# Kernel optimization log

Measured on AMD Instinct MI355X. Metric: run time of the kernel, lower is better.

The kernel has to match this reference:

```python
import jax, jax.numpy as jnp
import numpy as np

M, NC, NT, DX = 8, 1024, 512, 3
CHUNK = 512          # chunk_size
N_STEPS = 8          # n_steps (tol=0.0 -> torch early-stop never fires)
LR = 0.1
B1, B2, EPS = 0.9, 0.999, 1e-8
SQRT5 = 5.0 ** 0.5
LOG2PI = float(np.log(2.0 * np.pi))
NOISE_LB = 1e-4      # gpytorch GreaterThan(1e-4) noise constraint


def setup_inputs():
    key = jax.random.key(0)
    k1, k2, k3 = jax.random.split(key, 3)
    return {
        "xc": jax.random.normal(k1, (M, NC, DX), jnp.float32),
        "yc": jax.random.normal(k2, (M, NC, 1), jnp.float32),
        "xt": jax.random.normal(k3, (M, NT, DX), jnp.float32),
    }


def _kernel(x1, x2, ls, outscale):
    # ScaleKernel(MaternKernel(nu=2.5)); ls: [m,1,1], outscale: [m]
    xs1, xs2 = x1 / ls, x2 / ls
    d2 = (jnp.sum(xs1 * xs1, -1)[:, :, None]
          + jnp.sum(xs2 * xs2, -1)[:, None, :]
          - 2.0 * jnp.einsum('mnd,mkd->mnk', xs1, xs2))
    d2 = jnp.clip(d2, 1e-12, None)   # clamp like gpytorch dist for grad safety
    d = jnp.sqrt(d2)
    k = (1.0 + SQRT5 * d + (5.0 / 3.0) * d2) * jnp.exp(-SQRT5 * d)
    return outscale[:, None, None] * k


def _constrained(params):
    ls = jax.nn.softplus(params["raw_ls"])                          # [m,1,1]
    outscale = jax.nn.softplus(params["raw_os"])                    # [m]
    noise = jax.nn.softplus(params["raw_noise"][:, 0]) + NOISE_LB   # [m]
    return ls, outscale, noise


def _nll(params, x, y):
    # sum over tasks of -ExactMarginalLogLikelihood (gpytorch divides by n)
    ls, outscale, noise = _constrained(params)
    n = x.shape[1]
    K = _kernel(x, x, ls, outscale) + noise[:, None, None] * jnp.eye(n, dtype=x.dtype)
    L = jnp.linalg.cholesky(K)
    diff = y - params["const"][:, None]
    alpha = jax.scipy.linalg.cho_solve((L, True), diff[..., None])[..., 0]
    quad = jnp.sum(diff * alpha, -1)
    logdet = 2.0 * jnp.sum(jnp.log(jnp.diagonal(L, axis1=-2, axis2=-1)), -1)
    mll = -0.5 * (quad + logdet + n * LOG2PI) / n
    return jnp.sum(-mll)


def _adam_step(carry, x_sub, y_sub):
    p, m_, v_, t = carry
    g = jax.grad(_nll)(p, x_sub, y_sub)
    t = t + 1.0
    tm = jax.tree_util.tree_map
    m_ = tm(lambda a, gg: B1 * a + (1.0 - B1) * gg, m_, g)
    v_ = tm(lambda a, gg: B2 * a + (1.0 - B2) * gg * gg, v_, g)
    bc1 = 1.0 - B1 ** t
    bc2 = 1.0 - B2 ** t
    p = tm(lambda pp, mm, vv: pp - LR * (mm / bc1) / (jnp.sqrt(vv / bc2) + EPS), p, m_, v_)
    return (p, m_, v_, t)


def _gp_forward(xc, yc, xt):
    y = yc[..., 0]                                    # [m, nc]
    zl = lambda s: jnp.zeros(s, jnp.float32)
    # gpytorch raw params initialize to 0
    params = {"raw_ls": zl((M, 1, 1)), "raw_os": zl((M,)),
              "raw_noise": zl((M, 1)), "const": zl((M,))}
    m_ = jax.tree_util.tree_map(jnp.zeros_like, params)
    v_ = jax.tree_util.tree_map(jnp.zeros_like, params)
    carry = (params, m_, v_, jnp.float32(0.0))
    for i in range(0, NC, CHUNK):                     # 'Expanding' strategy
        end = min(i + CHUNK, NC)
        x_sub, y_sub = xc[:, :end], y[:, :end]
        step = lambda c, _: (_adam_step(c, x_sub, y_sub), None)
        carry, _ = jax.lax.scan(step, carry, None, length=N_STEPS)
    params = carry[0]
    # posterior predictive with trained hypers (train data = full context)
    ls, outscale, noise = _constrained(params)
    Kcc = _kernel(xc, xc, ls, outscale) + noise[:, None, None] * jnp.eye(NC, dtype=xc.dtype)
    L = jnp.linalg.cholesky(Kcc)
    diff = y - params["const"][:, None]
    alpha = jax.scipy.linalg.cho_solve((L, True), diff[..., None])[..., 0]
    Ktc = _kernel(xt, xc, ls, outscale)               # [m, nt, nc]
    mean = params["const"][:, None] + jnp.einsum('mtn,mn->mt', Ktc, alpha)
    v = jax.scipy.linalg.solve_triangular(L, jnp.swapaxes(Ktc, 1, 2), lower=True)  # [m,nc,nt]
    var_f = outscale[:, None] - jnp.sum(v * v, axis=1)  # Matern(0)=1 -> prior diag = outputscale
    var = var_f + noise[:, None]                      # likelihood(f) adds observation noise
    return jnp.stack([mean, var])                     # [2, m, nt]


def reference(xc, yc, xt):
    return _gp_forward(xc, yc, xt)
```

## Files before the change

### kernel.cpp

```cpp
#include <hip/hip_runtime.h>
#include <math.h>

constexpr int MM = 8;
constexpr int NC = 1024;
constexpr int NT = 512;

constexpr size_t OFF_A     = (size_t)MM * 1024 * 1024;
constexpr size_t OFF_T     = OFF_A * 2;
constexpr size_t OFF_KTC   = OFF_T + (size_t)MM * 512 * 512;
constexpr size_t OFF_ALPHA = OFF_KTC + (size_t)MM * NT * NC;
constexpr size_t OFF_SCAL  = OFF_ALPHA + (size_t)MM * 1024;
constexpr size_t OFF_ACC   = OFF_SCAL + (size_t)MM * 32;

#define S5 2.2360679775f

__device__ __forceinline__ float sigmf(float x) { return 1.0f / (1.0f + expf(-x)); }
__device__ __forceinline__ float softplusf(float x) { return fmaxf(x, 0.0f) + log1pf(expf(-fabsf(x))); }

__device__ __forceinline__ void lt_decode(int x, int& i, int& j) {
  int ii = 0;
  while ((ii + 1) * (ii + 2) / 2 <= x) ++ii;
  i = ii; j = x - ii * (ii + 1) / 2;
}

struct SMem {
  float Ls[64 * 65];
  float Us[64 * 65];
  float Tt[32 * 33];
  float dvec[64];
  float As[16][68];
  float Bs[16][68];
  float xi[64][3];
  float xj[64][3];
  float ai[64];
  float aj[64];
  float red[4][4];
};

template <int TA, int TB>
__device__ __forceinline__ void gemm64(const float* __restrict__ A, int lda,
                                       const float* __restrict__ B, int ldb,
                                       int kBeg, int kEnd, float acc[4][4], SMem& sm) {
  int tid = threadIdx.x, tx = tid & 15, ty = tid >> 4;
  float ra[4], rb[4];
  auto ldAB = [&](int k0) {
#pragma unroll
    for (int q = 0; q < 4; ++q) {
      int e = tid + (q << 8);
      if (TA) { int kk = e >> 6, r = e & 63; ra[q] = A[(size_t)(k0 + kk) * lda + r]; }
      else    { int r = e >> 4, kk = e & 15; ra[q] = A[(size_t)r * lda + k0 + kk]; }
      if (TB) { int c = e >> 4, kk = e & 15; rb[q] = B[(size_t)c * ldb + k0 + kk]; }
      else    { int kk = e >> 6, c = e & 63; rb[q] = B[(size_t)(k0 + kk) * ldb + c]; }
    }
  };
  ldAB(kBeg);
  for (int k0 = kBeg; k0 < kEnd; k0 += 16) {
    __syncthreads();
#pragma unroll
    for (int q = 0; q < 4; ++q) {
      int e = tid + (q << 8);
      if (TA) sm.As[e >> 6][e & 63] = ra[q]; else sm.As[e & 15][e >> 4] = ra[q];
      if (TB) sm.Bs[e & 15][e >> 4] = rb[q]; else sm.Bs[e >> 6][e & 63] = rb[q];
    }
    __syncthreads();
    if (k0 + 16 < kEnd) ldAB(k0 + 16);
#pragma unroll
    for (int kk = 0; kk < 16; ++kk) {
      float a[4], b[4];
#pragma unroll
      for (int i = 0; i < 4; ++i) a[i] = sm.As[kk][ty * 4 + i];
#pragma unroll
      for (int j = 0; j < 4; ++j) b[j] = sm.Bs[kk][tx * 4 + j];
#pragma unroll
      for (int i = 0; i < 4; ++i)
#pragma unroll
        for (int j = 0; j < 4; ++j) acc[i][j] = fmaf(a[i], b[j], acc[i][j]);
    }
  }
}

__device__ void factor64(SMem& sm, float* Uout, int ldu) {
  int tid = threadIdx.x;
  int tx = tid & 15, ty = tid >> 4;
  for (int j = 0; j < 63; ++j) {
    float rinv = 1.0f / sm.Ls[j * 65 + j];
    for (int i = j + 1 + ty; i < 64; i += 16) {
      float lij = sm.Ls[i * 65 + j] * rinv;
      for (int c = j + 1 + tx; c <= i; c += 16) sm.Ls[i * 65 + c] -= lij * sm.Ls[c * 65 + j];
    }
    __syncthreads();
  }
  if (tid < 64) sm.dvec[tid] = 1.0f / sqrtf(sm.Ls[tid * 65 + tid]);
  __syncthreads();
  for (int e = tid; e < 4096; e += 256) { int r = e >> 6, c = e & 63; if (c <= r) sm.Ls[r * 65 + c] *= sm.dvec[c]; }
  __syncthreads();
  for (int e = tid; e < 64 * 65; e += 256) sm.Us[e] = 0.0f;
  __syncthreads();
  if (tid < 64) {
    int b = tid >> 5, c0 = tid & 31, base = b * 32, gc = base + c0;
    sm.Us[gc * 65 + gc] = 1.0f / sm.Ls[gc * 65 + gc];
    for (int r = c0 + 1; r < 32; ++r) {
      int gr = base + r;
      float acc = 0.0f;
      for (int l = c0; l < r; ++l) acc += sm.Ls[gr * 65 + base + l] * sm.Us[(base + l) * 65 + gc];
      sm.Us[gr * 65 + gc] = -acc / sm.Ls[gr * 65 + gr];
    }
  }
  __syncthreads();
  for (int e = tid; e < 1024; e += 256) {
    int r = e >> 5, c = e & 31;
    float acc = 0.0f;
    for (int l = c; l < 32; ++l) acc += sm.Ls[(32 + r) * 65 + l] * sm.Us[l * 65 + c];
    sm.Tt[r * 33 + c] = acc;
  }
  __syncthreads();
  for (int e = tid; e < 1024; e += 256) {
    int r = e >> 5, c = e & 31;
    float acc = 0.0f;
    for (int l = 0; l <= r; ++l) acc += sm.Us[(32 + r) * 65 + 32 + l] * sm.Tt[l * 33 + c];
    sm.Us[(32 + r) * 65 + c] = -acc;
  }
  __syncthreads();
  for (int e = tid; e < 4096; e += 256) { int r = e >> 6, c = e & 63; Uout[(size_t)r * ldu + c] = sm.Us[r * 65 + c]; }
}


__global__ __launch_bounds__(256) void k_init(float* ws) {
  int t = threadIdx.x;
  float* scal = ws + OFF_SCAL;
  float* acc = ws + OFF_ACC;
  if (t < MM) {
    float* s = scal + t * 32;
    for (int i = 0; i < 12; ++i) s[i] = 0.0f;
    float sp0 = 0.69314718056f;
    s[12] = sp0; s[13] = sp0; s[14] = sp0 + 1e-4f; s[15] = 0.0f;
  }
  if (t < MM * 8) acc[t] = 0.0f;
}

__global__ __launch_bounds__(256) void k_adam(const float* __restrict__ yc, float* ws,
                                              int pn, int tstep) {
  int m = blockIdx.x, tid = threadIdx.x;
  float* sT = ws + OFF_SCAL + m * 32;
  float* accp = ws + OFF_ACC + m * 8;
  const float* al = ws + OFF_ALPHA + (size_t)m * 1024;
  const float* ym = yc + (size_t)m * NC;
  __shared__ float red[4][4];
  float cm = sT[15];
  float t4 = 0, t5 = 0, t6 = 0;
  for (int i = tid; i < pn; i += 256) {
    float a = al[i];
    t4 = fmaf(a, a, t4); t5 += a; t6 = fmaf(ym[i] - cm, a, t6);
  }
  for (int off = 32; off; off >>= 1) {
    t4 += __shfl_down(t4, off); t5 += __shfl_down(t5, off); t6 += __shfl_down(t6, off);
  }
  int wid = tid >> 6, lane = tid & 63;
  if (lane == 0) { red[wid][0] = t4; red[wid][1] = t5; red[wid][2] = t6; }
  __syncthreads();
  if (tid == 0) {
    t4 = red[0][0] + red[1][0] + red[2][0] + red[3][0];
    t5 = red[0][1] + red[1][1] + red[2][1] + red[3][1];
    t6 = red[0][2] + red[1][2] + red[2][2] + red[3][2];
    float T1 = accp[0], T2 = accp[1], t3 = accp[2];
    float ls = sT[12], os = sT[13], noi = sT[14];
    float fn = (float)pn;
    float g_ls = 0.5f / fn * (T1 - T2);
    float g_os = 0.5f / (fn * os) * (fn - noi * t3 - t6 + noi * t4);
    float g_no = 0.5f / fn * (t3 - t4);
    float g_c = -t5 / fn;
    float gr[4];
    gr[0] = g_ls * sigmf(sT[0]);
    gr[1] = g_os * sigmf(sT[1]);
    gr[2] = g_no * sigmf(sT[2]);
    gr[3] = g_c;
    float bc1 = 1.0f - powf(0.9f, (float)tstep);
    float bc2 = 1.0f - powf(0.999f, (float)tstep);
#pragma unroll
    for (int i = 0; i < 4; ++i) {
      float mv = 0.9f * sT[4 + i] + 0.1f * gr[i];
      float vv = 0.999f * sT[8 + i] + 0.001f * gr[i] * gr[i];
      sT[4 + i] = mv; sT[8 + i] = vv;
      sT[i] = sT[i] - 0.1f * (mv / bc1) / (sqrtf(vv / bc2) + 1e-8f);
    }
    sT[12] = softplusf(sT[0]);
    sT[13] = softplusf(sT[1]);
    sT[14] = softplusf(sT[2]) + 1e-4f;
    sT[15] = sT[3];
  }
}

__global__ __launch_bounds__(256) void k_buildK(const float* __restrict__ xc, float* ws, int n) {
  __shared__ SMem sm;
  int job = blockIdx.x, m = blockIdx.y, tid = threadIdx.x;
  const float* xm = xc + (size_t)m * NC * 3;
  float* Km = ws + (size_t)m * 1048576;
  float* Am = ws + OFF_A + (size_t)m * 1048576;
  const float* sT = ws + OFF_SCAL + m * 32;
  float ls = sT[12], os = sT[13], noi = sT[14];
  float il2 = 1.0f / (ls * ls);
  if (job >= 1 && job <= 4) {
    int zi = (job - 1) * 256 + tid;
    if (zi < n) ws[OFF_ALPHA + (size_t)m * 1024 + zi] = 0.0f;
  }
  if (job == 5 && tid < 4) ws[OFF_ACC + m * 8 + tid] = 0.0f;
  int bi, bj; lt_decode(job, bi, bj);
  if (tid < 64) {
    int r = bi * 64 + tid;
    sm.xi[tid][0] = xm[r * 3 + 0]; sm.xi[tid][1] = xm[r * 3 + 1]; sm.xi[tid][2] = xm[r * 3 + 2];
  } else if (tid < 128) {
    int lr = tid - 64; int r = bj * 64 + lr;
    sm.xj[lr][0] = xm[r * 3 + 0]; sm.xj[lr][1] = xm[r * 3 + 1]; sm.xj[lr][2] = xm[r * 3 + 2];
  }
  __syncthreads();
  if (job == 0) {
    for (int e = tid; e < 4096; e += 256) {
      int r = e >> 6, c = e & 63;
      float d0 = sm.xi[r][0] - sm.xj[c][0], d1 = sm.xi[r][1] - sm.xj[c][1], d2 = sm.xi[r][2] - sm.xj[c][2];
      float r2 = d0 * d0 + d1 * d1 + d2 * d2;
      float z = fmaxf(r2 * il2, 1e-12f);
      float dd = sqrtf(z);
      float kv = os * (1.0f + S5 * dd + (5.0f / 3.0f) * z) * expf(-S5 * dd);
      if (r == c) kv += noi;
      sm.Ls[r * 65 + c] = kv;
    }
    __syncthreads();
    factor64(sm, Am, n);
  } else {
    for (int e = tid; e < 4096; e += 256) {
      int r = e >> 6, c = e & 63;
      float d0 = sm.xi[r][0] - sm.xj[c][0], d1 = sm.xi[r][1] - sm.xj[c][1], d2 = sm.xi[r][2] - sm.xj[c][2];
      float r2 = d0 * d0 + d1 * d1 + d2 * d2;
      float z = fmaxf(r2 * il2, 1e-12f);
      float dd = sqrtf(z);
      float kv = os * (1.0f + S5 * dd + (5.0f / 3.0f) * z) * expf(-S5 * dd);
      if (bi == bj && r == c) kv += noi;
      Km[(size_t)(bi * 64 + r) * n + bj * 64 + c] = kv;
    }
  }
}

__global__ __launch_bounds__(256) void k_trail(float* ws, int k, int n) {
  __shared__ SMem sm;
  int job = blockIdx.x, m = blockIdx.y, tid = threadIdx.x;
  int tx = tid & 15, ty = tid >> 4;
  float* Km = ws + (size_t)m * 1048576;
  float* Am = ws + OFF_A + (size_t)m * 1048576;
  const float* Linv = Am + (size_t)(k * 64) * n + k * 64;
  int di, dj; lt_decode(job, di, dj);
  int i = k + 1 + di, j = k + 1 + dj;
  float pp[4][4] = {};
  gemm64<0, 1>(Km + (size_t)(i * 64) * n + k * 64, n, Linv, n, 0, 64, pp, sm);
  __syncthreads();
#pragma unroll
  for (int ii = 0; ii < 4; ++ii)
#pragma unroll
    for (int jj = 0; jj < 4; ++jj) sm.Ls[(ty * 4 + ii) * 65 + tx * 4 + jj] = pp[ii][jj];
  if (di == dj) {
    float* P = Am + (size_t)(i * 64) * n + k * 64;
#pragma unroll
    for (int ii = 0; ii < 4; ++ii)
#pragma unroll
      for (int jj = 0; jj < 4; ++jj) P[(size_t)(ty * 4 + ii) * n + tx * 4 + jj] = pp[ii][jj];
  } else {
#pragma unroll
    for (int ii = 0; ii < 4; ++ii)
#pragma unroll
      for (int jj = 0; jj < 4; ++jj) pp[ii][jj] = 0.0f;
    gemm64<0, 1>(Km + (size_t)(j * 64) * n + k * 64, n, Linv, n, 0, 64, pp, sm);
#pragma unroll
    for (int ii = 0; ii < 4; ++ii)
#pragma unroll
      for (int jj = 0; jj < 4; ++jj) sm.Us[(ty * 4 + ii) * 65 + tx * 4 + jj] = pp[ii][jj];
  }
  __syncthreads();
  float acc[4][4] = {};
  {
    const float* Bsrc = (di == dj) ? sm.Ls : sm.Us;
    for (int l = 0; l < 64; ++l) {
      float a[4], b[4];
#pragma unroll
      for (int ii = 0; ii < 4; ++ii) a[ii] = sm.Ls[(ty * 4 + ii) * 65 + l];
#pragma unroll
      for (int jj = 0; jj < 4; ++jj) b[jj] = Bsrc[(tx * 4 + jj) * 65 + l];
#pragma unroll
      for (int ii = 0; ii < 4; ++ii)
#pragma unroll
        for (int jj = 0; jj < 4; ++jj) acc[ii][jj] = fmaf(a[ii], b[jj], acc[ii][jj]);
    }
  }
  float* C = Km + (size_t)(i * 64) * n + j * 64;
  if (job == 0) {
    __syncthreads();
#pragma unroll
    for (int ii = 0; ii < 4; ++ii)
#pragma unroll
      for (int jj = 0; jj < 4; ++jj)
        sm.Ls[(ty * 4 + ii) * 65 + tx * 4 + jj] =
            C[(size_t)(ty * 4 + ii) * n + tx * 4 + jj] - acc[ii][jj];
    __syncthreads();
    factor64(sm, Am + (size_t)((k + 1) * 64) * n + (k + 1) * 64, n);
  } else {
#pragma unroll
    for (int ii = 0; ii < 4; ++ii)
#pragma unroll
      for (int jj = 0; jj < 4; ++jj)
        C[(size_t)(ty * 4 + ii) * n + tx * 4 + jj] -= acc[ii][jj];
  }
}

__global__ __launch_bounds__(256) void k_trinv64(float* ws, int n) {
  __shared__ SMem sm;
  int p = blockIdx.x, m = blockIdx.y, tid = threadIdx.x;
  int tx = tid & 15, ty = tid >> 4;
  float* Am = ws + OFF_A + (size_t)m * 1048576;
  int rb = (2 * p + 1) * 64, cb = 2 * p * 64;
  for (int e = tid; e < 4096; e += 256) {
    int r = e >> 6, c = e & 63;
    sm.Ls[r * 65 + c] = Am[(size_t)(rb + r) * n + cb + c];
    sm.Us[r * 65 + c] = Am[(size_t)(cb + r) * n + cb + c];
  }
  __syncthreads();
  float tt[4][4] = {};
  for (int l = 0; l < 64; ++l) {
    float a[4], b[4];
#pragma unroll
    for (int ii = 0; ii < 4; ++ii) a[ii] = sm.Ls[(ty * 4 + ii) * 65 + l];
#pragma unroll
    for (int jj = 0; jj < 4; ++jj) b[jj] = sm.Us[l * 65 + tx * 4 + jj];
#pragma unroll
    for (int ii = 0; ii < 4; ++ii)
#pragma unroll
      for (int jj = 0; jj < 4; ++jj) tt[ii][jj] = fmaf(a[ii], b[jj], tt[ii][jj]);
  }
  __syncthreads();
#pragma unroll
  for (int ii = 0; ii < 4; ++ii)
#pragma unroll
    for (int jj = 0; jj < 4; ++jj) sm.Ls[(ty * 4 + ii) * 65 + tx * 4 + jj] = tt[ii][jj];
  for (int e = tid; e < 4096; e += 256) {
    int r = e >> 6, c = e & 63;
    sm.Us[r * 65 + c] = Am[(size_t)(rb + r) * n + rb + c];
  }
  __syncthreads();
  float oo[4][4] = {};
  for (int l = 0; l < 64; ++l) {
    float a[4], b[4];
#pragma unroll
    for (int ii = 0; ii < 4; ++ii) a[ii] = sm.Us[(ty * 4 + ii) * 65 + l];
#pragma unroll
    for (int jj = 0; jj < 4; ++jj) b[jj] = sm.Ls[l * 65 + tx * 4 + jj];
#pragma unroll
    for (int ii = 0; ii < 4; ++ii)
#pragma unroll
      for (int jj = 0; jj < 4; ++jj) oo[ii][jj] = fmaf(a[ii], b[jj], oo[ii][jj]);
  }
#pragma unroll
  for (int ii = 0; ii < 4; ++ii)
#pragma unroll
    for (int jj = 0; jj < 4; ++jj)
      Am[(size_t)(rb + ty * 4 + ii) * n + cb + tx * 4 + jj] = -oo[ii][jj];
}

__global__ __launch_bounds__(256) void k_trinvT(float* ws, int s, int n) {
  __shared__ SMem sm;
  int job = blockIdx.x, m = blockIdx.y;
  int tx = threadIdx.x & 15, ty = threadIdx.x >> 4;
  float* Am = ws + OFF_A + (size_t)m * 1048576;
  float* Tm = ws + OFF_T + (size_t)m * 262144;
  int st = s >> 6;
  int p = job / (st * st), rem = job % (st * st);
  int ti = rem / st, tj = rem % st;
  int base = p * 2 * s;
  float acc[4][4] = {};
  gemm64<0, 0>(Am + (size_t)(base + s + ti * 64) * n + base, n,
               Am + (size_t)base * n + base + tj * 64, n, tj * 64, s, acc, sm);
  float* C = Tm + (size_t)p * s * s + (size_t)(ti * 64) * s + tj * 64;
#pragma unroll
  for (int ii = 0; ii < 4; ++ii)
#pragma unroll
    for (int jj = 0; jj < 4; ++jj) C[(size_t)(ty * 4 + ii) * s + tx * 4 + jj] = acc[ii][jj];
}

__global__ __launch_bounds__(256) void k_trinvA(float* ws, int s, int n) {
  __shared__ SMem sm;
  int job = blockIdx.x, m = blockIdx.y;
  int tx = threadIdx.x & 15, ty = threadIdx.x >> 4;
  float* Am = ws + OFF_A + (size_t)m * 1048576;
  const float* Tm = ws + OFF_T + (size_t)m * 262144;
  int st = s >> 6;
  int p = job / (st * st), rem = job % (st * st);
  int ti = rem / st, tj = rem % st;
  int base = p * 2 * s;
  float acc[4][4] = {};
  gemm64<0, 0>(Am + (size_t)(base + s + ti * 64) * n + base + s, n,
               Tm + (size_t)p * s * s + tj * 64, s, 0, (ti + 1) * 64, acc, sm);
  float* C = Am + (size_t)(base + s + ti * 64) * n + base + tj * 64;
#pragma unroll
  for (int ii = 0; ii < 4; ++ii)
#pragma unroll
    for (int jj = 0; jj < 4; ++jj) C[(size_t)(ty * 4 + ii) * n + tx * 4 + jj] = -acc[ii][jj];
}

__global__ __launch_bounds__(256) void k_syrkAT(const float* __restrict__ yc, float* ws, int n) {
  __shared__ SMem sm;
  int job = blockIdx.x, m = blockIdx.y, tid = threadIdx.x;
  int tx = tid & 15, ty = tid >> 4;
  const float* Am = ws + OFF_A + (size_t)m * 1048576;
  float* Gm = ws + (size_t)m * 1048576;
  const float* ym = yc + (size_t)m * NC;
  float* accp = ws + OFF_ACC + m * 8;
  float* al = ws + OFF_ALPHA + (size_t)m * 1024;
  float cm = ws[OFF_SCAL + m * 32 + 15];
  int ib, jb; lt_decode(job, ib, jb);
  if (tid < 64) sm.ai[tid] = ym[ib * 64 + tid] - cm;
  else if (tid < 128) sm.aj[tid - 64] = ym[jb * 64 + tid - 64] - cm;
  float acc[4][4] = {};
  gemm64<1, 0>(Am + ib * 64, n, Am + jb * 64, n, ib * 64, n, acc, sm);
#pragma unroll
  for (int ii = 0; ii < 4; ++ii)
#pragma unroll
    for (int jj = 0; jj < 4; ++jj) {
      int r = ty * 4 + ii, c = tx * 4 + jj;
      Gm[(size_t)(ib * 64 + r) * n + jb * 64 + c] = acc[ii][jj];
      if (ib != jb) Gm[(size_t)(jb * 64 + c) * n + ib * 64 + r] = acc[ii][jj];
    }
  if (ib == jb && tx == ty) {
    atomicAdd(&accp[2], acc[0][0] + acc[1][1] + acc[2][2] + acc[3][3]);
  }
  float rowp[4];
#pragma unroll
  for (int i = 0; i < 4; ++i) {
    float s = 0.0f;
#pragma unroll
    for (int j = 0; j < 4; ++j) s = fmaf(acc[i][j], sm.aj[tx * 4 + j], s);
    rowp[i] = s;
  }
  float colp[4];
  if (ib != jb) {
#pragma unroll
    for (int j = 0; j < 4; ++j) {
      float s = 0.0f;
#pragma unroll
      for (int i = 0; i < 4; ++i) s = fmaf(acc[i][j], sm.ai[ty * 4 + i], s);
      colp[j] = s;
    }
  }
  __syncthreads();
  float* redA = &sm.As[0][0];
  float* redB = &sm.Bs[0][0];
#pragma unroll
  for (int i = 0; i < 4; ++i) redA[(ty * 4 + i) * 16 + tx] = rowp[i];
  if (ib != jb) {
#pragma unroll
    for (int j = 0; j < 4; ++j) redB[(tx * 4 + j) * 16 + ty] = colp[j];
  }
  __syncthreads();
  if (tid < 64) {
    float s = 0.0f;
#pragma unroll
    for (int q = 0; q < 16; ++q) s += redA[tid * 16 + q];
    atomicAdd(&al[ib * 64 + tid], s);
    if (ib != jb) {
      float s2 = 0.0f;
#pragma unroll
      for (int q = 0; q < 16; ++q) s2 += redB[tid * 16 + q];
      atomicAdd(&al[jb * 64 + tid], s2);
    }
  }
}

__global__ __launch_bounds__(256) void k_reduce(const float* __restrict__ xc, float* ws, int n) {
  __shared__ SMem sm;
  int job = blockIdx.x, m = blockIdx.y, tid = threadIdx.x;
  const float* xm = xc + (size_t)m * NC * 3;
  const float* Gm = ws + (size_t)m * 1048576;
  const float* al = ws + OFF_ALPHA + (size_t)m * 1024;
  float* accp = ws + OFF_ACC + m * 8;
  const float* sT = ws + OFF_SCAL + m * 32;
  float ls = sT[12], os = sT[13];
  float il2 = 1.0f / (ls * ls);
  float c53 = (5.0f / 3.0f) * os / ls;
  int bi, bj; lt_decode(job, bi, bj);
  float w = (bi == bj) ? 1.0f : 2.0f;
  if (tid < 64) {
    int r = bi * 64 + tid;
    sm.xi[tid][0] = xm[r * 3 + 0]; sm.xi[tid][1] = xm[r * 3 + 1]; sm.xi[tid][2] = xm[r * 3 + 2];
    sm.ai[tid] = al[r];
  } else if (tid < 128) {
    int lr = tid - 64; int r = bj * 64 + lr;
    sm.xj[lr][0] = xm[r * 3 + 0]; sm.xj[lr][1] = xm[r * 3 + 1]; sm.xj[lr][2] = xm[r * 3 + 2];
    sm.aj[lr] = al[r];
  }
  __syncthreads();
  float a1 = 0.0f, a2 = 0.0f;
  for (int e = tid; e < 4096; e += 256) {
    int r = e >> 6, c = e & 63;
    float d0 = sm.xi[r][0] - sm.xj[c][0], d1 = sm.xi[r][1] - sm.xj[c][1], d2 = sm.xi[r][2] - sm.xj[c][2];
    float r2 = d0 * d0 + d1 * d1 + d2 * d2;
    float z = fmaxf(r2 * il2, 1e-12f);
    float dd = sqrtf(z);
    float Cv = c53 * z * (1.0f + S5 * dd) * expf(-S5 * dd);
    float g = Gm[(size_t)(bi * 64 + r) * n + bj * 64 + c];
    a1 = fmaf(g, Cv, a1);
    a2 = fmaf(sm.ai[r] * sm.aj[c], Cv, a2);
  }
  a1 *= w; a2 *= w;
  for (int off = 32; off; off >>= 1) { a1 += __shfl_down(a1, off); a2 += __shfl_down(a2, off); }
  int wid = tid >> 6, lane = tid & 63;
  if (lane == 0) { sm.red[wid][0] = a1; sm.red[wid][1] = a2; }
  __syncthreads();
  if (tid == 0) {
    a1 = sm.red[0][0] + sm.red[1][0] + sm.red[2][0] + sm.red[3][0];
    a2 = sm.red[0][1] + sm.red[1][1] + sm.red[2][1] + sm.red[3][1];
    atomicAdd(&accp[0], a1);
    atomicAdd(&accp[1], a2);
  }
}

__global__ __launch_bounds__(256) void k_buildKtc(const float* __restrict__ xt,
                                                  const float* __restrict__ xc, float* ws) {
  __shared__ SMem sm;
  int job = blockIdx.x, m = blockIdx.y, tid = threadIdx.x;
  const float* xtm = xt + (size_t)m * NT * 3;
  const float* xm = xc + (size_t)m * NC * 3;
  float* Kt = ws + OFF_KTC + (size_t)m * NT * NC;
  float* Tm = ws + OFF_T + (size_t)m * 262144;
  const float* sT = ws + OFF_SCAL + m * 32;
  float ls = sT[12], os = sT[13];
  float il2 = 1.0f / (ls * ls);
  if (job < 2) {
    int z = job * 256 + tid;
    Tm[z] = 0.0f; Tm[NT + z] = 0.0f;
  }
  int ti = job >> 4, tj = job & 15;
  if (tid < 64) {
    int r = ti * 64 + tid;
    sm.xi[tid][0] = xtm[r * 3 + 0]; sm.xi[tid][1] = xtm[r * 3 + 1]; sm.xi[tid][2] = xtm[r * 3 + 2];
  } else if (tid < 128) {
    int lr = tid - 64; int r = tj * 64 + lr;
    sm.xj[lr][0] = xm[r * 3 + 0]; sm.xj[lr][1] = xm[r * 3 + 1]; sm.xj[lr][2] = xm[r * 3 + 2];
  }
  __syncthreads();
  for (int e = tid; e < 4096; e += 256) {
    int r = e >> 6, c = e & 63;
    float d0 = sm.xi[r][0] - sm.xj[c][0], d1 = sm.xi[r][1] - sm.xj[c][1], d2 = sm.xi[r][2] - sm.xj[c][2];
    float r2 = d0 * d0 + d1 * d1 + d2 * d2;
    float z = fmaxf(r2 * il2, 1e-12f);
    float dd = sqrtf(z);
    float kv = os * (1.0f + S5 * dd + (5.0f / 3.0f) * z) * expf(-S5 * dd);
    Kt[(size_t)(ti * 64 + r) * NC + tj * 64 + c] = kv;
  }
}

__global__ __launch_bounds__(256) void k_predW(float* ws) {
  __shared__ SMem sm;
  int job = blockIdx.x, m = blockIdx.y, tid = threadIdx.x;
  int tx = tid & 15, ty = tid >> 4;
  const float* Kt = ws + OFF_KTC + (size_t)m * NT * NC;
  const float* Gm = ws + (size_t)m * 1048576;
  const float* al = ws + OFF_ALPHA + (size_t)m * 1024;
  float* S1 = ws + OFF_T + (size_t)m * 262144;
  float* S2 = S1 + NT;
  int ti = job >> 4, tj = job & 15;
  if (tid < 64) sm.aj[tid] = al[tj * 64 + tid];
  float acc[4][4] = {};
  gemm64<0, 0>(Kt + (size_t)(ti * 64) * NC, NC, Gm + tj * 64, 1024, 0, 1024, acc, sm);
  float s1p[4], s2p[4];
#pragma unroll
  for (int i = 0; i < 4; ++i) {
    float a1 = 0.0f, a2 = 0.0f;
    const float* kr = Kt + (size_t)(ti * 64 + ty * 4 + i) * NC + tj * 64;
#pragma unroll
    for (int j = 0; j < 4; ++j) {
      float kv = kr[tx * 4 + j];
      a1 = fmaf(kv, sm.aj[tx * 4 + j], a1);
      a2 = fmaf(kv, acc[i][j], a2);
    }
    s1p[i] = a1; s2p[i] = a2;
  }
  __syncthreads();
  float* redA = &sm.As[0][0];
  float* redB = &sm.Bs[0][0];
#pragma unroll
  for (int i = 0; i < 4; ++i) {
    redA[(ty * 4 + i) * 16 + tx] = s1p[i];
    redB[(ty * 4 + i) * 16 + tx] = s2p[i];
  }
  __syncthreads();
  if (tid < 64) {
    float a1 = 0.0f, a2 = 0.0f;
#pragma unroll
    for (int q = 0; q < 16; ++q) { a1 += redA[tid * 16 + q]; a2 += redB[tid * 16 + q]; }
    atomicAdd(&S1[ti * 64 + tid], a1);
    atomicAdd(&S2[ti * 64 + tid], a2);
  }
}

__global__ __launch_bounds__(256) void k_final(float* ws, float* out) {
  int m = blockIdx.y, t = blockIdx.x * 256 + threadIdx.x;
  const float* S1 = ws + OFF_T + (size_t)m * 262144;
  const float* S2 = S1 + NT;
  const float* sT = ws + OFF_SCAL + m * 32;
  if (t < NT) {
    out[(size_t)m * NT + t] = sT[15] + S1[t];
    out[(size_t)MM * NT + (size_t)m * NT + t] = sT[13] + sT[14] - S2[t];
  }
}

extern "C" void kernel_launch(void* const* d_in, const int* in_sizes, int n_in,
                              void* d_out, int out_size, void* d_ws, size_t ws_size,
                              hipStream_t stream) {
  const float* xc = (const float*)d_in[0];
  const float* yc = (const float*)d_in[1];
  const float* xt = (const float*)d_in[2];
  float* out = (float*)d_out;
  float* ws = (float*)d_ws;

  k_init<<<dim3(1), dim3(256), 0, stream>>>(ws);

  for (int step = 0; step < 17; ++step) {
    int n = step < 8 ? 512 : 1024;
    int nb = n >> 6;
    if (step > 0) {
      int pn = step <= 8 ? 512 : 1024;
      k_adam<<<dim3(MM), dim3(256), 0, stream>>>(yc, ws, pn, step);
    }
    k_buildK<<<dim3(nb * (nb + 1) / 2, MM), dim3(256), 0, stream>>>(xc, ws, n);
    for (int k = 0; k <= nb - 2; ++k) {
      int t = nb - 1 - k;
      k_trail<<<dim3(t * (t + 1) / 2, MM), dim3(256), 0, stream>>>(ws, k, n);
    }
    k_trinv64<<<dim3(n / 128, MM), dim3(256), 0, stream>>>(ws, n);
    for (int s = 128; s < n; s <<= 1) {
      int st = s >> 6, np = n / (2 * s);
      k_trinvT<<<dim3(np * st * st, MM), dim3(256), 0, stream>>>(ws, s, n);
      k_trinvA<<<dim3(np * st * st, MM), dim3(256), 0, stream>>>(ws, s, n);
    }
    k_syrkAT<<<dim3(nb * (nb + 1) / 2, MM), dim3(256), 0, stream>>>(yc, ws, n);
    if (step < 16) {
      k_reduce<<<dim3(nb * (nb + 1) / 2, MM), dim3(256), 0, stream>>>(xc, ws, n);
    }
  }

  k_buildKtc<<<dim3(128, MM), dim3(256), 0, stream>>>(xt, xc, ws);
  k_predW<<<dim3(128, MM), dim3(256), 0, stream>>>(ws);
  k_final<<<dim3(2, MM), dim3(256), 0, stream>>>(ws, out);

  (void)in_sizes; (void)n_in; (void)out_size; (void)ws_size;
}
```

Before: 19.79 ms.

## Fuse syrk, gradient reduction and Adam update; use 128 tiles and explicit alpha solve

The separate syrk, reduce and Adam kernels become one kernel built on 128x128 GEMM tiles. It computes the gradient contributions straight from the accumulator tile without writing G during training, and a last-block ticket counter runs the Adam update. Alpha is now computed by two matrix-vector kernels instead of atomics inside the syrk. The triangular-inverse GEMMs and the prediction GEMM also move to 128 tiles, and expf is replaced by __expf. The aim is fewer launches and less memory traffic, at the cost of fewer blocks per launch, higher register pressure, and some loss of precision from the fast exp.

```diff
diff --git a/kernel.cpp b/kernel.cpp
--- a/kernel.cpp
+++ b/kernel.cpp
@@ -11,6 +11,7 @@
 constexpr size_t OFF_ALPHA = OFF_KTC + (size_t)MM * NT * NC;
 constexpr size_t OFF_SCAL  = OFF_ALPHA + (size_t)MM * 1024;
 constexpr size_t OFF_ACC   = OFF_SCAL + (size_t)MM * 32;
+constexpr size_t OFF_CTR   = OFF_ACC + (size_t)MM * 8;
 
 #define S5 2.2360679775f
 
@@ -37,6 +38,16 @@
   float red[4][4];
 };
 
+struct SMem128 {
+  float As[16][132];
+  float Bs[16][132];
+  float xi[128][3];
+  float xj[128][3];
+  float ai[128];
+  float aj[128];
+  float red[4][4];
+};
+
 template <int TA, int TB>
 __device__ __forceinline__ void gemm64(const float* __restrict__ A, int lda,
                                        const float* __restrict__ B, int ldb,
@@ -75,6 +86,48 @@
       for (int i = 0; i < 4; ++i)
 #pragma unroll
         for (int j = 0; j < 4; ++j) acc[i][j] = fmaf(a[i], b[j], acc[i][j]);
+    }
+  }
+}
+
+template <int TA, int TB>
+__device__ __forceinline__ void gemm128(const float* __restrict__ A, int lda,
+                                        const float* __restrict__ B, int ldb,
+                                        int kBeg, int kEnd, float acc[8][8], SMem128& sm) {
+  int tid = threadIdx.x, tx = tid & 15, ty = tid >> 4;
+  float ra[8], rb[8];
+  auto ldAB = [&](int k0) {
+#pragma unroll
+    for (int q = 0; q < 8; ++q) {
+      int e = tid + (q << 8);
+      if (TA) { int kk = e >> 7, r = e & 127; ra[q] = A[(size_t)(k0 + kk) * lda + r]; }
+      else    { int r = e >> 4, kk = e & 15;  ra[q] = A[(size_t)r * lda + k0 + kk]; }
+      if (TB) { int c = e >> 4, kk = e & 15;  rb[q] = B[(size_t)c * ldb + k0 + kk]; }
+      else    { int kk = e >> 7, c = e & 127; rb[q] = B[(size_t)(k0 + kk) * ldb + c]; }
+    }
+  };
+  ldAB(kBeg);
+  for (int k0 = kBeg; k0 < kEnd; k0 += 16) {
+    __syncthreads();
+#pragma unroll
+    for (int q = 0; q < 8; ++q) {
+      int e = tid + (q << 8);
+      if (TA) sm.As[e >> 7][e & 127] = ra[q]; else sm.As[e & 15][e >> 4] = ra[q];
+      if (TB) sm.Bs[e & 15][e >> 4] = rb[q];  else sm.Bs[e >> 7][e & 127] = rb[q];
+    }
+    __syncthreads();
+    if (k0 + 16 < kEnd) ldAB(k0 + 16);
+#pragma unroll
+    for (int kk = 0; kk < 16; ++kk) {
+      float a[8], b[8];
+#pragma unroll
+      for (int i = 0; i < 8; ++i) a[i] = sm.As[kk][ty * 8 + i];
+#pragma unroll
+      for (int j = 0; j < 8; ++j) b[j] = sm.Bs[kk][tx * 8 + j];
+#pragma unroll
+      for (int i = 0; i < 8; ++i)
+#pragma unroll
+        for (int j = 0; j < 8; ++j) acc[i][j] = fmaf(a[i], b[j], acc[i][j]);
     }
   }
 }
@@ -128,66 +181,14 @@
 __global__ __launch_bounds__(256) void k_init(float* ws) {
   int t = threadIdx.x;
   float* scal = ws + OFF_SCAL;
-  float* acc = ws + OFF_ACC;
   if (t < MM) {
     float* s = scal + t * 32;
     for (int i = 0; i < 12; ++i) s[i] = 0.0f;
     float sp0 = 0.69314718056f;
     s[12] = sp0; s[13] = sp0; s[14] = sp0 + 1e-4f; s[15] = 0.0f;
   }
-  if (t < MM * 8) acc[t] = 0.0f;
-}
-
-__global__ __launch_bounds__(256) void k_adam(const float* __restrict__ yc, float* ws,
-                                              int pn, int tstep) {
-  int m = blockIdx.x, tid = threadIdx.x;
-  float* sT = ws + OFF_SCAL + m * 32;
-  float* accp = ws + OFF_ACC + m * 8;
-  const float* al = ws + OFF_ALPHA + (size_t)m * 1024;
-  const float* ym = yc + (size_t)m * NC;
-  __shared__ float red[4][4];
-  float cm = sT[15];
-  float t4 = 0, t5 = 0, t6 = 0;
-  for (int i = tid; i < pn; i += 256) {
-    float a = al[i];
-    t4 = fmaf(a, a, t4); t5 += a; t6 = fmaf(ym[i] - cm, a, t6);
-  }
-  for (int off = 32; off; off >>= 1) {
-    t4 += __shfl_down(t4, off); t5 += __shfl_down(t5, off); t6 += __shfl_down(t6, off);
-  }
-  int wid = tid >> 6, lane = tid & 63;
-  if (lane == 0) { red[wid][0] = t4; red[wid][1] = t5; red[wid][2] = t6; }
-  __syncthreads();
-  if (tid == 0) {
-    t4 = red[0][0] + red[1][0] + red[2][0] + red[3][0];
-    t5 = red[0][1] + red[1][1] + red[2][1] + red[3][1];
-    t6 = red[0][2] + red[1][2] + red[2][2] + red[3][2];
-    float T1 = accp[0], T2 = accp[1], t3 = accp[2];
-    float ls = sT[12], os = sT[13], noi = sT[14];
-    float fn = (float)pn;
-    float g_ls = 0.5f / fn * (T1 - T2);
-    float g_os = 0.5f / (fn * os) * (fn - noi * t3 - t6 + noi * t4);
-    float g_no = 0.5f / fn * (t3 - t4);
-    float g_c = -t5 / fn;
-    float gr[4];
-    gr[0] = g_ls * sigmf(sT[0]);
-    gr[1] = g_os * sigmf(sT[1]);
-    gr[2] = g_no * sigmf(sT[2]);
-    gr[3] = g_c;
-    float bc1 = 1.0f - powf(0.9f, (float)tstep);
-    float bc2 = 1.0f - powf(0.999f, (float)tstep);
-#pragma unroll
-    for (int i = 0; i < 4; ++i) {
-      float mv = 0.9f * sT[4 + i] + 0.1f * gr[i];
-      float vv = 0.999f * sT[8 + i] + 0.001f * gr[i] * gr[i];
-      sT[4 + i] = mv; sT[8 + i] = vv;
-      sT[i] = sT[i] - 0.1f * (mv / bc1) / (sqrtf(vv / bc2) + 1e-8f);
-    }
-    sT[12] = softplusf(sT[0]);
-    sT[13] = softplusf(sT[1]);
-    sT[14] = softplusf(sT[2]) + 1e-4f;
-    sT[15] = sT[3];
-  }
+  if (t < MM * 8) ws[OFF_ACC + t] = 0.0f;
+  if (t < MM) ((unsigned*)(ws + OFF_CTR))[t] = 0u;
 }
 
 __global__ __launch_bounds__(256) void k_buildK(const float* __restrict__ xc, float* ws, int n) {
@@ -199,11 +200,10 @@
   const float* sT = ws + OFF_SCAL + m * 32;
   float ls = sT[12], os = sT[13], noi = sT[14];
   float il2 = 1.0f / (ls * ls);
-  if (job >= 1 && job <= 4) {
-    int zi = (job - 1) * 256 + tid;
-    if (zi < n) ws[OFF_ALPHA + (size_t)m * 1024 + zi] = 0.0f;
-  }
-  if (job == 5 && tid < 4) ws[OFF_ACC + m * 8 + tid] = 0.0f;
+  if (job == 5) {
+    if (tid < 3) ws[OFF_ACC + m * 8 + tid] = 0.0f;
+    if (tid == 3) ((unsigned*)(ws + OFF_CTR))[m] = 0u;
+  }
   int bi, bj; lt_decode(job, bi, bj);
   if (tid < 64) {
     int r = bi * 64 + tid;
@@ -220,7 +220,7 @@
       float r2 = d0 * d0 + d1 * d1 + d2 * d2;
       float z = fmaxf(r2 * il2, 1e-12f);
       float dd = sqrtf(z);
-      float kv = os * (1.0f + S5 * dd + (5.0f / 3.0f) * z) * expf(-S5 * dd);
+      float kv = os * (1.0f + S5 * dd + (5.0f / 3.0f) * z) * __expf(-S5 * dd);
       if (r == c) kv += noi;
       sm.Ls[r * 65 + c] = kv;
     }
@@ -233,7 +233,7 @@
       float r2 = d0 * d0 + d1 * d1 + d2 * d2;
       float z = fmaxf(r2 * il2, 1e-12f);
       float dd = sqrtf(z);
-      float kv = os * (1.0f + S5 * dd + (5.0f / 3.0f) * z) * expf(-S5 * dd);
+      float kv = os * (1.0f + S5 * dd + (5.0f / 3.0f) * z) * __expf(-S5 * dd);
       if (bi == bj && r == c) kv += noi;
       Km[(size_t)(bi * 64 + r) * n + bj * 64 + c] = kv;
     }
@@ -319,6 +319,7 @@
     int r = e >> 6, c = e & 63;
     sm.Ls[r * 65 + c] = Am[(size_t)(rb + r) * n + cb + c];
     sm.Us[r * 65 + c] = Am[(size_t)(cb + r) * n + cb + c];
+    Am[(size_t)(cb + r) * n + rb + c] = 0.0f;
   }
   __syncthreads();
   float tt[4][4] = {};
@@ -363,158 +364,212 @@
 }
 
 __global__ __launch_bounds__(256) void k_trinvT(float* ws, int s, int n) {
-  __shared__ SMem sm;
+  __shared__ SMem128 sm;
   int job = blockIdx.x, m = blockIdx.y;
   int tx = threadIdx.x & 15, ty = threadIdx.x >> 4;
   float* Am = ws + OFF_A + (size_t)m * 1048576;
   float* Tm = ws + OFF_T + (size_t)m * 262144;
-  int st = s >> 6;
+  int st = s >> 7;
   int p = job / (st * st), rem = job % (st * st);
   int ti = rem / st, tj = rem % st;
   int base = p * 2 * s;
-  float acc[4][4] = {};
-  gemm64<0, 0>(Am + (size_t)(base + s + ti * 64) * n + base, n,
-               Am + (size_t)base * n + base + tj * 64, n, tj * 64, s, acc, sm);
-  float* C = Tm + (size_t)p * s * s + (size_t)(ti * 64) * s + tj * 64;
-#pragma unroll
-  for (int ii = 0; ii < 4; ++ii)
-#pragma unroll
-    for (int jj = 0; jj < 4; ++jj) C[(size_t)(ty * 4 + ii) * s + tx * 4 + jj] = acc[ii][jj];
+  float acc[8][8] = {};
+  gemm128<0, 0>(Am + (size_t)(base + s + ti * 128) * n + base, n,
+                Am + (size_t)base * n + base + tj * 128, n, tj * 128, s, acc, sm);
+  float* C = Tm + (size_t)p * s * s + (size_t)(ti * 128) * s + tj * 128;
+#pragma unroll
+  for (int ii = 0; ii < 8; ++ii)
+#pragma unroll
+    for (int jj = 0; jj < 8; ++jj) C[(size_t)(ty * 8 + ii) * s + tx * 8 + jj] = acc[ii][jj];
 }
 
 __global__ __launch_bounds__(256) void k_trinvA(float* ws, int s, int n) {
-  __shared__ SMem sm;
+  __shared__ SMem128 sm;
   int job = blockIdx.x, m = blockIdx.y;
   int tx = threadIdx.x & 15, ty = threadIdx.x >> 4;
   float* Am = ws + OFF_A + (size_t)m * 1048576;
   const float* Tm = ws + OFF_T + (size_t)m * 262144;
-  int st = s >> 6;
+  int st = s >> 7;
   int p = job / (st * st), rem = job % (st * st);
   int ti = rem / st, tj = rem % st;
   int base = p * 2 * s;
-  float acc[4][4] = {};
-  gemm64<0, 0>(Am + (size_t)(base + s + ti * 64) * n + base + s, n,
-               Tm + (size_t)p * s * s + tj * 64, s, 0, (ti + 1) * 64, acc, sm);
-  float* C = Am + (size_t)(base + s + ti * 64) * n + base + tj * 64;
-#pragma unroll
-  for (int ii = 0; ii < 4; ++ii)
-#pragma unroll
-    for (int jj = 0; jj < 4; ++jj) C[(size_t)(ty * 4 + ii) * n + tx * 4 + jj] = -acc[ii][jj];
-}
-
-__global__ __launch_bounds__(256) void k_syrkAT(const float* __restrict__ yc, float* ws, int n) {
-  __shared__ SMem sm;
+  float acc[8][8] = {};
+  gemm128<0, 0>(Am + (size_t)(base + s + ti * 128) * n + base + s, n,
+                Tm + (size_t)p * s * s + tj * 128, s, 0, (ti + 1) * 128, acc, sm);
+  float* C = Am + (size_t)(base + s + ti * 128) * n + base + tj * 128;
+#pragma unroll
+  for (int ii = 0; ii < 8; ++ii)
+#pragma unroll
+    for (int jj = 0; jj < 8; ++jj) C[(size_t)(ty * 8 + ii) * n + tx * 8 + jj] = -acc[ii][jj];
+}
+
+__global__ __launch_bounds__(256) void k_alpha1(const float* __restrict__ yc, float* ws, int n) {
+  int m = blockIdx.y, tid = threadIdx.x;
+  int r0 = blockIdx.x * 64;
+  int w = tid >> 6, lane = tid & 63;
+  const float* Am = ws + OFF_A + (size_t)m * 1048576;
+  const float* ym = yc + (size_t)m * NC;
+  float* v = ws + OFF_T + (size_t)m * 262144;
+  float cm = ws[OFF_SCAL + m * 32 + 15];
+  for (int rr = 0; rr < 16; ++rr) {
+    int i = r0 + rr * 4 + w;
+    float sum = 0.0f;
+    const float* row = Am + (size_t)i * n;
+    for (int j = lane; j <= i; j += 64) sum = fmaf(row[j], ym[j] - cm, sum);
+    for (int off = 32; off; off >>= 1) sum += __shfl_down(sum, off);
+    if (lane == 0) v[i] = sum;
+  }
+}
+
+__global__ __launch_bounds__(256) void k_alpha2(float* ws, int n) {
+  __shared__ float red2[4][64];
+  int m = blockIdx.y, tid = threadIdx.x;
+  int c0 = blockIdx.x * 64;
+  int w = tid >> 6, lane = tid & 63;
+  const float* Am = ws + OFF_A + (size_t)m * 1048576;
+  const float* v = ws + OFF_T + (size_t)m * 262144;
+  float* al = ws + OFF_ALPHA + (size_t)m * 1024;
+  int j = c0 + lane;
+  float part = 0.0f;
+  for (int i = c0 + w; i < n; i += 4) {
+    float vi = v[i];
+    if (j <= i) part = fmaf(Am[(size_t)i * n + j], vi, part);
+  }
+  red2[w][lane] = part;
+  __syncthreads();
+  if (tid < 64) al[c0 + tid] = red2[0][tid] + red2[1][tid] + red2[2][tid] + red2[3][tid];
+}
+
+__global__ __launch_bounds__(256) void k_syrkATR(const float* __restrict__ yc,
+                                                 const float* __restrict__ xc,
+                                                 float* ws, int n, int step) {
+  __shared__ SMem128 sm;
+  __shared__ unsigned tkt;
   int job = blockIdx.x, m = blockIdx.y, tid = threadIdx.x;
   int tx = tid & 15, ty = tid >> 4;
   const float* Am = ws + OFF_A + (size_t)m * 1048576;
   float* Gm = ws + (size_t)m * 1048576;
+  float* sT = ws + OFF_SCAL + m * 32;
+  float* accp = ws + OFF_ACC + m * 8;
+  const float* al = ws + OFF_ALPHA + (size_t)m * 1024;
+  const float* xm = xc + (size_t)m * NC * 3;
   const float* ym = yc + (size_t)m * NC;
-  float* accp = ws + OFF_ACC + m * 8;
-  float* al = ws + OFF_ALPHA + (size_t)m * 1024;
-  float cm = ws[OFF_SCAL + m * 32 + 15];
+  int train = (step < 16);
+  int nb128 = n >> 7;
+  int njobs = nb128 * (nb128 + 1) / 2;
   int ib, jb; lt_decode(job, ib, jb);
-  if (tid < 64) sm.ai[tid] = ym[ib * 64 + tid] - cm;
-  else if (tid < 128) sm.aj[tid - 64] = ym[jb * 64 + tid - 64] - cm;
-  float acc[4][4] = {};
-  gemm64<1, 0>(Am + ib * 64, n, Am + jb * 64, n, ib * 64, n, acc, sm);
-#pragma unroll
-  for (int ii = 0; ii < 4; ++ii)
-#pragma unroll
-    for (int jj = 0; jj < 4; ++jj) {
-      int r = ty * 4 + ii, c = tx * 4 + jj;
-      Gm[(size_t)(ib * 64 + r) * n + jb * 64 + c] = acc[ii][jj];
-      if (ib != jb) Gm[(size_t)(jb * 64 + c) * n + ib * 64 + r] = acc[ii][jj];
-    }
-  if (ib == jb && tx == ty) {
-    atomicAdd(&accp[2], acc[0][0] + acc[1][1] + acc[2][2] + acc[3][3]);
-  }
-  float rowp[4];
-#pragma unroll
-  for (int i = 0; i < 4; ++i) {
-    float s = 0.0f;
-#pragma unroll
-    for (int j = 0; j < 4; ++j) s = fmaf(acc[i][j], sm.aj[tx * 4 + j], s);
-    rowp[i] = s;
-  }
-  float colp[4];
-  if (ib != jb) {
-#pragma unroll
-    for (int j = 0; j < 4; ++j) {
-      float s = 0.0f;
-#pragma unroll
-      for (int i = 0; i < 4; ++i) s = fmaf(acc[i][j], sm.ai[ty * 4 + i], s);
-      colp[j] = s;
-    }
-  }
-  __syncthreads();
-  float* redA = &sm.As[0][0];
-  float* redB = &sm.Bs[0][0];
-#pragma unroll
-  for (int i = 0; i < 4; ++i) redA[(ty * 4 + i) * 16 + tx] = rowp[i];
-  if (ib != jb) {
-#pragma unroll
-    for (int j = 0; j < 4; ++j) redB[(tx * 4 + j) * 16 + ty] = colp[j];
-  }
-  __syncthreads();
-  if (tid < 64) {
-    float s = 0.0f;
-#pragma unroll
-    for (int q = 0; q < 16; ++q) s += redA[tid * 16 + q];
-    atomicAdd(&al[ib * 64 + tid], s);
-    if (ib != jb) {
-      float s2 = 0.0f;
-#pragma unroll
-      for (int q = 0; q < 16; ++q) s2 += redB[tid * 16 + q];
-      atomicAdd(&al[jb * 64 + tid], s2);
-    }
-  }
-}
-
-__global__ __launch_bounds__(256) void k_reduce(const float* __restrict__ xc, float* ws, int n) {
-  __shared__ SMem sm;
-  int job = blockIdx.x, m = blockIdx.y, tid = threadIdx.x;
-  const float* xm = xc + (size_t)m * NC * 3;
-  const float* Gm = ws + (size_t)m * 1048576;
-  const float* al = ws + OFF_ALPHA + (size_t)m * 1024;
-  float* accp = ws + OFF_ACC + m * 8;
-  const float* sT = ws + OFF_SCAL + m * 32;
   float ls = sT[12], os = sT[13];
+  if (train) {
+    if (tid < 128) {
+      int r = ib * 128 + tid;
+      sm.xi[tid][0] = xm[r * 3 + 0]; sm.xi[tid][1] = xm[r * 3 + 1]; sm.xi[tid][2] = xm[r * 3 + 2];
+      sm.ai[tid] = al[r];
+    } else {
+      int lr = tid - 128; int r = jb * 128 + lr;
+      sm.xj[lr][0] = xm[r * 3 + 0]; sm.xj[lr][1] = xm[r * 3 + 1]; sm.xj[lr][2] = xm[r * 3 + 2];
+      sm.aj[lr] = al[r];
+    }
+  }
+  float acc[8][8] = {};
+  gemm128<1, 0>(Am + ib * 128, n, Am + jb * 128, n, ib * 128, n, acc, sm);
+  if (!train) {
+#pragma unroll
+    for (int ii = 0; ii < 8; ++ii)
+#pragma unroll
+      for (int jj = 0; jj < 8; ++jj) {
+        int r = ty * 8 + ii, c = tx * 8 + jj;
+        Gm[(size_t)(ib * 128 + r) * n + jb * 128 + c] = acc[ii][jj];
+        if (ib != jb) Gm[(size_t)(jb * 128 + c) * n + ib * 128 + r] = acc[ii][jj];
+      }
+    return;
+  }
   float il2 = 1.0f / (ls * ls);
   float c53 = (5.0f / 3.0f) * os / ls;
-  int bi, bj; lt_decode(job, bi, bj);
-  float w = (bi == bj) ? 1.0f : 2.0f;
-  if (tid < 64) {
-    int r = bi * 64 + tid;
-    sm.xi[tid][0] = xm[r * 3 + 0]; sm.xi[tid][1] = xm[r * 3 + 1]; sm.xi[tid][2] = xm[r * 3 + 2];
-    sm.ai[tid] = al[r];
-  } else if (tid < 128) {
-    int lr = tid - 64; int r = bj * 64 + lr;
-    sm.xj[lr][0] = xm[r * 3 + 0]; sm.xj[lr][1] = xm[r * 3 + 1]; sm.xj[lr][2] = xm[r * 3 + 2];
-    sm.aj[lr] = al[r];
-  }
-  __syncthreads();
-  float a1 = 0.0f, a2 = 0.0f;
-  for (int e = tid; e < 4096; e += 256) {
-    int r = e >> 6, c = e & 63;
-    float d0 = sm.xi[r][0] - sm.xj[c][0], d1 = sm.xi[r][1] - sm.xj[c][1], d2 = sm.xi[r][2] - sm.xj[c][2];
-    float r2 = d0 * d0 + d1 * d1 + d2 * d2;
-    float z = fmaxf(r2 * il2, 1e-12f);
-    float dd = sqrtf(z);
-    float Cv = c53 * z * (1.0f + S5 * dd) * expf(-S5 * dd);
-    float g = Gm[(size_t)(bi * 64 + r) * n + bj * 64 + c];
-    a1 = fmaf(g, Cv, a1);
-    a2 = fmaf(sm.ai[r] * sm.aj[c], Cv, a2);
+  float w = (ib == jb) ? 1.0f : 2.0f;
+  float a1 = 0.0f, a2 = 0.0f, a3 = 0.0f;
+#pragma unroll
+  for (int ii = 0; ii < 8; ++ii) {
+    int r = ty * 8 + ii;
+    float x0 = sm.xi[r][0], x1 = sm.xi[r][1], x2 = sm.xi[r][2], ar = sm.ai[r];
+#pragma unroll
+    for (int jj = 0; jj < 8; ++jj) {
+      int c = tx * 8 + jj;
+      float d0 = x0 - sm.xj[c][0], d1 = x1 - sm.xj[c][1], d2 = x2 - sm.xj[c][2];
+      float r2 = d0 * d0 + d1 * d1 + d2 * d2;
+      float z = fmaxf(r2 * il2, 1e-12f);
+      float dd = sqrtf(z);
+      float Cv = c53 * z * (1.0f + S5 * dd) * __expf(-S5 * dd);
+      a1 = fmaf(acc[ii][jj], Cv, a1);
+      a2 = fmaf(ar * sm.aj[c], Cv, a2);
+    }
+    if (ib == jb && tx == ty) a3 += acc[ii][ii];
   }
   a1 *= w; a2 *= w;
-  for (int off = 32; off; off >>= 1) { a1 += __shfl_down(a1, off); a2 += __shfl_down(a2, off); }
+  for (int off = 32; off; off >>= 1) {
+    a1 += __shfl_down(a1, off); a2 += __shfl_down(a2, off); a3 += __shfl_down(a3, off);
+  }
   int wid = tid >> 6, lane = tid & 63;
-  if (lane == 0) { sm.red[wid][0] = a1; sm.red[wid][1] = a2; }
+  __syncthreads();
+  if (lane == 0) { sm.red[wid][0] = a1; sm.red[wid][1] = a2; sm.red[wid][2] = a3; }
   __syncthreads();
   if (tid == 0) {
     a1 = sm.red[0][0] + sm.red[1][0] + sm.red[2][0] + sm.red[3][0];
     a2 = sm.red[0][1] + sm.red[1][1] + sm.red[2][1] + sm.red[3][1];
+    a3 = sm.red[0][2] + sm.red[1][2] + sm.red[2][2] + sm.red[3][2];
     atomicAdd(&accp[0], a1);
     atomicAdd(&accp[1], a2);
+    if (ib == jb) atomicAdd(&accp[2], a3);
+  }
+  __threadfence();
+  if (tid == 0)
+    tkt = __hip_atomic_fetch_add((unsigned*)(ws + OFF_CTR) + m, 1u,
+                                 __ATOMIC_ACQ_REL, __HIP_MEMORY_SCOPE_AGENT);
+  __syncthreads();
+  if (tkt != (unsigned)(njobs - 1)) return;
+  float cm = sT[15];
+  float t4 = 0, t5 = 0, t6 = 0;
+  for (int i = tid; i < n; i += 256) {
+    float a = al[i];
+    t4 = fmaf(a, a, t4); t5 += a; t6 = fmaf(ym[i] - cm, a, t6);
+  }
+  for (int off = 32; off; off >>= 1) {
+    t4 += __shfl_down(t4, off); t5 += __shfl_down(t5, off); t6 += __shfl_down(t6, off);
+  }
+  __syncthreads();
+  if (lane == 0) { sm.red[wid][0] = t4; sm.red[wid][1] = t5; sm.red[wid][2] = t6; }
+  __syncthreads();
+  if (tid == 0) {
+    t4 = sm.red[0][0] + sm.red[1][0] + sm.red[2][0] + sm.red[3][0];
+    t5 = sm.red[0][1] + sm.red[1][1] + sm.red[2][1] + sm.red[3][1];
+    t6 = sm.red[0][2] + sm.red[1][2] + sm.red[2][2] + sm.red[3][2];
+    float T1 = __hip_atomic_fetch_add(&accp[0], 0.0f, __ATOMIC_RELAXED, __HIP_MEMORY_SCOPE_AGENT);
+    float T2 = __hip_atomic_fetch_add(&accp[1], 0.0f, __ATOMIC_RELAXED, __HIP_MEMORY_SCOPE_AGENT);
+    float t3 = __hip_atomic_fetch_add(&accp[2], 0.0f, __ATOMIC_RELAXED, __HIP_MEMORY_SCOPE_AGENT);
+    float noi = sT[14];
+    float fn = (float)n;
+    float g_ls = 0.5f / fn * (T1 - T2);
+    float g_os = 0.5f / (fn * os) * (fn - noi * t3 - t6 + noi * t4);
+    float g_no = 0.5f / fn * (t3 - t4);
+    float g_c = -t5 / fn;
+    float gr[4];
+    gr[0] = g_ls * sigmf(sT[0]);
+    gr[1] = g_os * sigmf(sT[1]);
+    gr[2] = g_no * sigmf(sT[2]);
+    gr[3] = g_c;
+    int tstep = step + 1;
+    float bc1 = 1.0f - powf(0.9f, (float)tstep);
+    float bc2 = 1.0f - powf(0.999f, (float)tstep);
+#pragma unroll
+    for (int i = 0; i < 4; ++i) {
+      float mv = 0.9f * sT[4 + i] + 0.1f * gr[i];
+      float vv = 0.999f * sT[8 + i] + 0.001f * gr[i] * gr[i];
+      sT[4 + i] = mv; sT[8 + i] = vv;
+      sT[i] = sT[i] - 0.1f * (mv / bc1) / (sqrtf(vv / bc2) + 1e-8f);
+    }
+    sT[12] = softplusf(sT[0]);
+    sT[13] = softplusf(sT[1]);
+    sT[14] = softplusf(sT[2]) + 1e-4f;
+    sT[15] = sT[3];
   }
 }
 
@@ -548,13 +603,13 @@
     float r2 = d0 * d0 + d1 * d1 + d2 * d2;
     float z = fmaxf(r2 * il2, 1e-12f);
     float dd = sqrtf(z);
-    float kv = os * (1.0f + S5 * dd + (5.0f / 3.0f) * z) * expf(-S5 * dd);
+    float kv = os * (1.0f + S5 * dd + (5.0f / 3.0f) * z) * __expf(-S5 * dd);
     Kt[(size_t)(ti * 64 + r) * NC + tj * 64 + c] = kv;
   }
 }
 
 __global__ __launch_bounds__(256) void k_predW(float* ws) {
-  __shared__ SMem sm;
+  __shared__ SMem128 sm;
   int job = blockIdx.x, m = blockIdx.y, tid = threadIdx.x;
   int tx = tid & 15, ty = tid >> 4;
   const float* Kt = ws + OFF_KTC + (size_t)m * NT * NC;
@@ -562,38 +617,38 @@
   const float* al = ws + OFF_ALPHA + (size_t)m * 1024;
   float* S1 = ws + OFF_T + (size_t)m * 262144;
   float* S2 = S1 + NT;
-  int ti = job >> 4, tj = job & 15;
-  if (tid < 64) sm.aj[tid] = al[tj * 64 + tid];
-  float acc[4][4] = {};
-  gemm64<0, 0>(Kt + (size_t)(ti * 64) * NC, NC, Gm + tj * 64, 1024, 0, 1024, acc, sm);
-  float s1p[4], s2p[4];
-#pragma unroll
-  for (int i = 0; i < 4; ++i) {
+  int ti = job >> 3, tj = job & 7;
+  if (tid < 128) sm.ai[tid] = al[tj * 128 + tid];
+  float acc[8][8] = {};
+  gemm128<0, 0>(Kt + (size_t)(ti * 128) * NC, NC, Gm + tj * 128, 1024, 0, 1024, acc, sm);
+  float s1p[8], s2p[8];
+#pragma unroll
+  for (int ii = 0; ii < 8; ++ii) {
     float a1 = 0.0f, a2 = 0.0f;
-    const float* kr = Kt + (size_t)(ti * 64 + ty * 4 + i) * NC + tj * 64;
-#pragma unroll
-    for (int j = 0; j < 4; ++j) {
-      float kv = kr[tx * 4 + j];
-      a1 = fmaf(kv, sm.aj[tx * 4 + j], a1);
-      a2 = fmaf(kv, acc[i][j], a2);
-    }
-    s1p[i] = a1; s2p[i] = a2;
+    const float* kr = Kt + (size_t)(ti * 128 + ty * 8 + ii) * NC + tj * 128;
+#pragma unroll
+    for (int jj = 0; jj < 8; ++jj) {
+      float kv = kr[tx * 8 + jj];
+      a1 = fmaf(kv, sm.ai[tx * 8 + jj], a1);
+      a2 = fmaf(kv, acc[ii][jj], a2);
+    }
+    s1p[ii] = a1; s2p[ii] = a2;
   }
   __syncthreads();
   float* redA = &sm.As[0][0];
   float* redB = &sm.Bs[0][0];
 #pragma unroll
-  for (int i = 0; i < 4; ++i) {
-    redA[(ty * 4 + i) * 16 + tx] = s1p[i];
-    redB[(ty * 4 + i) * 16 + tx] = s2p[i];
-  }
-  __syncthreads();
-  if (tid < 64) {
+  for (int ii = 0; ii < 8; ++ii) {
+    redA[(ty * 8 + ii) * 16 + tx] = s1p[ii];
+    redB[(ty * 8 + ii) * 16 + tx] = s2p[ii];
+  }
+  __syncthreads();
+  if (tid < 128) {
     float a1 = 0.0f, a2 = 0.0f;
 #pragma unroll
     for (int q = 0; q < 16; ++q) { a1 += redA[tid * 16 + q]; a2 += redB[tid * 16 + q]; }
-    atomicAdd(&S1[ti * 64 + tid], a1);
-    atomicAdd(&S2[ti * 64 + tid], a2);
+    atomicAdd(&S1[ti * 128 + tid], a1);
+    atomicAdd(&S2[ti * 128 + tid], a2);
   }
 }
 
@@ -622,10 +677,6 @@
   for (int step = 0; step < 17; ++step) {
     int n = step < 8 ? 512 : 1024;
     int nb = n >> 6;
-    if (step > 0) {
-      int pn = step <= 8 ? 512 : 1024;
-      k_adam<<<dim3(MM), dim3(256), 0, stream>>>(yc, ws, pn, step);
-    }
     k_buildK<<<dim3(nb * (nb + 1) / 2, MM), dim3(256), 0, stream>>>(xc, ws, n);
     for (int k = 0; k <= nb - 2; ++k) {
       int t = nb - 1 - k;
@@ -633,18 +684,18 @@
     }
     k_trinv64<<<dim3(n / 128, MM), dim3(256), 0, stream>>>(ws, n);
     for (int s = 128; s < n; s <<= 1) {
-      int st = s >> 6, np = n / (2 * s);
+      int st = s >> 7, np = n / (2 * s);
       k_trinvT<<<dim3(np * st * st, MM), dim3(256), 0, stream>>>(ws, s, n);
       k_trinvA<<<dim3(np * st * st, MM), dim3(256), 0, stream>>>(ws, s, n);
     }
-    k_syrkAT<<<dim3(nb * (nb + 1) / 2, MM), dim3(256), 0, stream>>>(yc, ws, n);
-    if (step < 16) {
-      k_reduce<<<dim3(nb * (nb + 1) / 2, MM), dim3(256), 0, stream>>>(xc, ws, n);
-    }
+    k_alpha1<<<dim3(n / 64, MM), dim3(256), 0, stream>>>(yc, ws, n);
+    k_alpha2<<<dim3(n / 64, MM), dim3(256), 0, stream>>>(ws, n);
+    int nb128 = n >> 7;
+    k_syrkATR<<<dim3(nb128 * (nb128 + 1) / 2, MM), dim3(256), 0, stream>>>(yc, xc, ws, n, step);
   }
 
   k_buildKtc<<<dim3(128, MM), dim3(256), 0, stream>>>(xt, xc, ws);
-  k_predW<<<dim3(128, MM), dim3(256), 0, stream>>>(ws);
+  k_predW<<<dim3(32, MM), dim3(256), 0, stream>>>(ws);
   k_final<<<dim3(2, MM), dim3(256), 0, stream>>>(ws, out);
 
   (void)in_sizes; (void)n_in; (void)out_size; (void)ws_size;
```

After: 25.22 ms. 27.4% more time.
